# Optimization experiments

Measured on AMD Instinct MI355X. Metric: run time of the kernel, lower is better.

Reference implementation:

```python
import jax, jax.numpy as jnp
import numpy as np

NUM_PARTITIONS = 128
C = 32
D = 128
B, S, K = 4, 2048, 2


def setup_inputs() -> dict:
    key = jax.random.key(0)
    k1, k2, k3, k4 = jax.random.split(key, 4)
    partition_indices = jax.random.randint(k1, (B, S, K), 0, NUM_PARTITIONS)
    keys = jax.random.normal(k2, (B, S, K, C), dtype=jnp.float32)
    values = jax.random.normal(k3, (B, S, D), dtype=jnp.float32)
    queries = jax.random.normal(k4, (B, S, D), dtype=jnp.float32)
    return {
        "partition_indices": partition_indices,
        "keys": keys,
        "values": values,
        "queries": queries,
    }


def reference(partition_indices, keys, values, queries):
    # States start at zero; update() scatter-adds outer(k_bti, v_bt) into
    # states[p_bti]. read() then computes sum_i states[p_bti].mean(axis=0) * q_bt.
    b, s, k, c = keys.shape
    d = values.shape[-1]
    # outer products: [B,S,K,c,d]
    outer = keys[..., :, None] * values[:, :, None, None, :]
    flat_outer = outer.reshape(b * s * k, c, d)
    seg = partition_indices.reshape(-1)
    # scatter-add into partitioned states [P, c, d]
    states = jax.ops.segment_sum(flat_outer, seg, num_segments=NUM_PARTITIONS)
    means = states.mean(axis=1)  # [P, d]
    gathered = means[partition_indices]  # [B, S, K, d]
    out = gathered.sum(axis=2) * queries  # [B, S, d]
    return out
```

## Files before the change

### kernel.cpp

```cpp
#include <hip/hip_runtime.h>
#include <hip/hip_bf16.h>

#define P_  128
#define C_  32
#define D_  128
#define BS_ 8192
#define PD_ (P_*D_)
#define NB_MAX 256

__global__ __launch_bounds__(256) void scatter_partials(
    const int* __restrict__ idx, const float* __restrict__ keys,
    const float* __restrict__ values, float* __restrict__ partials,
    int rowsPerBlk)
{
    __shared__ float lmeans[PD_];
    const int tid  = threadIdx.x;
    for (int i = tid; i < PD_; i += 256) lmeans[i] = 0.f;
    __syncthreads();

    const int lane = tid & 63;
    const int wave = tid >> 6;
    const int r0 = blockIdx.x * rowsPerBlk;
    int r1 = r0 + rowsPerBlk; if (r1 > BS_) r1 = BS_;

    for (int r = r0 + wave; r < r1; r += 4) {
        const float kv = keys[(size_t)r * 64 + lane];
        const int i0 = idx[r * 2 + 0];
        const int i1 = idx[r * 2 + 1];
        const float va = values[(size_t)r * D_ + lane];
        const float vb = values[(size_t)r * D_ + 64 + lane];
        float s = kv;
        s += __shfl_xor(s, 16);
        s += __shfl_xor(s, 8);
        s += __shfl_xor(s, 4);
        s += __shfl_xor(s, 2);
        s += __shfl_xor(s, 1);
        const float ks0 = __shfl(s, 0)  * (1.f / 32.f);
        const float ks1 = __shfl(s, 32) * (1.f / 32.f);
        atomicAdd(&lmeans[i0 * D_ + lane],      ks0 * va);
        atomicAdd(&lmeans[i0 * D_ + 64 + lane], ks0 * vb);
        atomicAdd(&lmeans[i1 * D_ + lane],      ks1 * va);
        atomicAdd(&lmeans[i1 * D_ + 64 + lane], ks1 * vb);
    }
    __syncthreads();

    float4* dst = (float4*)(partials + (size_t)blockIdx.x * PD_);
    const float4* src = (const float4*)lmeans;
    for (int i = tid; i < PD_ / 4; i += 256) dst[i] = src[i];
}

__global__ __launch_bounds__(256) void reduce_partials(
    const float* __restrict__ partials, float* __restrict__ means, int nb)
{
    const int i = blockIdx.x * 256 + threadIdx.x;
    float s = 0.f;
    #pragma unroll 8
    for (int b = 0; b < nb; ++b) s += partials[(size_t)b * PD_ + i];
    means[i] = s;
}

__global__ __launch_bounds__(256) void emit_out(
    const int* __restrict__ idx, const float* __restrict__ means,
    const float* __restrict__ queries, float* __restrict__ out)
{
    const int gid = blockIdx.x * 256 + threadIdx.x;
    const int row = gid >> 5;
    const int d4  = gid & 31;
    const int i0 = idx[row * 2 + 0];
    const int i1 = idx[row * 2 + 1];
    const float4 q = ((const float4*)queries)[gid];
    const float4* m4 = (const float4*)means;
    const float4 a = m4[i0 * 32 + d4];
    const float4 b = m4[i1 * 32 + d4];
    float4 o;
    o.x = (a.x + b.x) * q.x;
    o.y = (a.y + b.y) * q.y;
    o.z = (a.z + b.z) * q.z;
    o.w = (a.w + b.w) * q.w;
    ((float4*)out)[gid] = o;
}

extern "C" void kernel_launch(void* const* d_in, const int* in_sizes, int n_in,
                              void* d_out, int out_size, void* d_ws, size_t ws_size,
                              hipStream_t stream) {
    const int*   idx     = (const int*)d_in[0];
    const float* keys    = (const float*)d_in[1];
    const float* values  = (const float*)d_in[2];
    const float* queries = (const float*)d_in[3];
    float* out = (float*)d_out;
    float* ws = (float*)d_ws;

    size_t slots = ws_size / (PD_ * sizeof(float));
    int nb = (int)slots - 1;
    if (nb > NB_MAX) nb = NB_MAX;
    if (nb < 1)      nb = 1;
    float* partials = ws;
    float* means    = ws + (size_t)nb * PD_;
    const int rowsPerBlk = (BS_ + nb - 1) / nb;

    scatter_partials<<<nb, 256, 0, stream>>>(idx, keys, values, partials, rowsPerBlk);
    reduce_partials<<<PD_ / 256, 256, 0, stream>>>(partials, means, nb);
    emit_out<<<(BS_ * D_ / 4) / 256, 256, 0, stream>>>(idx, means, queries, out);
}
```

Measured before the change: 105.1 us.

## Fix block count, batch row loads in scatter, split partial reduction across waves

Hardcodes 256 scatter blocks of 512 threads (8 waves), each wave loading its 4 rows up front so the global loads are in flight together before the LDS atomics. The reduce kernel now gives each element four waves, each summing 64 partials, and combines them in shared memory, which raises memory-level parallelism across 4x more blocks. Index loads are vectorised as int2. Dropping the workspace-size check assumes the workspace always holds 257 PD slots, and that may fail if it is smaller.

```diff
diff --git a/kernel.cpp b/kernel.cpp
--- a/kernel.cpp
+++ b/kernel.cpp
@@ -6,30 +6,36 @@
 #define D_  128
 #define BS_ 8192
 #define PD_ (P_*D_)
-#define NB_MAX 256
+#define NB_ 256
 
-__global__ __launch_bounds__(256) void scatter_partials(
+__global__ __launch_bounds__(512) void scatter_partials(
     const int* __restrict__ idx, const float* __restrict__ keys,
-    const float* __restrict__ values, float* __restrict__ partials,
-    int rowsPerBlk)
+    const float* __restrict__ values, float* __restrict__ partials)
 {
     __shared__ float lmeans[PD_];
-    const int tid  = threadIdx.x;
-    for (int i = tid; i < PD_; i += 256) lmeans[i] = 0.f;
+    float4* lm4 = (float4*)lmeans;
+    const int tid = threadIdx.x;
+    for (int i = tid; i < PD_ / 4; i += 512) lm4[i] = float4{0.f, 0.f, 0.f, 0.f};
     __syncthreads();
 
     const int lane = tid & 63;
     const int wave = tid >> 6;
-    const int r0 = blockIdx.x * rowsPerBlk;
-    int r1 = r0 + rowsPerBlk; if (r1 > BS_) r1 = BS_;
+    const int rbase = blockIdx.x * 32 + wave;
 
-    for (int r = r0 + wave; r < r1; r += 4) {
-        const float kv = keys[(size_t)r * 64 + lane];
-        const int i0 = idx[r * 2 + 0];
-        const int i1 = idx[r * 2 + 1];
-        const float va = values[(size_t)r * D_ + lane];
-        const float vb = values[(size_t)r * D_ + 64 + lane];
-        float s = kv;
+    float kv[4], va[4], vb[4];
+    int2  ii[4];
+    #pragma unroll
+    for (int j = 0; j < 4; ++j) {
+        const int r = rbase + 8 * j;
+        kv[j] = keys[(size_t)r * 64 + lane];
+        ii[j] = ((const int2*)idx)[r];
+        va[j] = values[(size_t)r * D_ + lane];
+        vb[j] = values[(size_t)r * D_ + 64 + lane];
+    }
+
+    #pragma unroll
+    for (int j = 0; j < 4; ++j) {
+        float s = kv[j];
         s += __shfl_xor(s, 16);
         s += __shfl_xor(s, 8);
         s += __shfl_xor(s, 4);
@@ -37,26 +43,33 @@
         s += __shfl_xor(s, 1);
         const float ks0 = __shfl(s, 0)  * (1.f / 32.f);
         const float ks1 = __shfl(s, 32) * (1.f / 32.f);
-        atomicAdd(&lmeans[i0 * D_ + lane],      ks0 * va);
-        atomicAdd(&lmeans[i0 * D_ + 64 + lane], ks0 * vb);
-        atomicAdd(&lmeans[i1 * D_ + lane],      ks1 * va);
-        atomicAdd(&lmeans[i1 * D_ + 64 + lane], ks1 * vb);
+        atomicAdd(&lmeans[ii[j].x * D_ + lane],      ks0 * va[j]);
+        atomicAdd(&lmeans[ii[j].x * D_ + 64 + lane], ks0 * vb[j]);
+        atomicAdd(&lmeans[ii[j].y * D_ + lane],      ks1 * va[j]);
+        atomicAdd(&lmeans[ii[j].y * D_ + 64 + lane], ks1 * vb[j]);
     }
     __syncthreads();
 
     float4* dst = (float4*)(partials + (size_t)blockIdx.x * PD_);
-    const float4* src = (const float4*)lmeans;
-    for (int i = tid; i < PD_ / 4; i += 256) dst[i] = src[i];
+    for (int i = tid; i < PD_ / 4; i += 512) dst[i] = lm4[i];
 }
 
 __global__ __launch_bounds__(256) void reduce_partials(
-    const float* __restrict__ partials, float* __restrict__ means, int nb)
+    const float* __restrict__ partials, float* __restrict__ means)
 {
-    const int i = blockIdx.x * 256 + threadIdx.x;
+    __shared__ float red[4][64];
+    const int t  = threadIdx.x;
+    const int el = t & 63;
+    const int g  = t >> 6;
+    const int e  = blockIdx.x * 64 + el;
     float s = 0.f;
     #pragma unroll 8
-    for (int b = 0; b < nb; ++b) s += partials[(size_t)b * PD_ + i];
-    means[i] = s;
+    for (int j = 0; j < 64; ++j)
+        s += partials[(size_t)(g * 64 + j) * PD_ + e];
+    red[g][el] = s;
+    __syncthreads();
+    if (t < 64)
+        means[blockIdx.x * 64 + t] = red[0][t] + red[1][t] + red[2][t] + red[3][t];
 }
 
 __global__ __launch_bounds__(256) void emit_out(
@@ -66,12 +79,11 @@
     const int gid = blockIdx.x * 256 + threadIdx.x;
     const int row = gid >> 5;
     const int d4  = gid & 31;
-    const int i0 = idx[row * 2 + 0];
-    const int i1 = idx[row * 2 + 1];
+    const int2 ii = ((const int2*)idx)[row];
     const float4 q = ((const float4*)queries)[gid];
     const float4* m4 = (const float4*)means;
-    const float4 a = m4[i0 * 32 + d4];
-    const float4 b = m4[i1 * 32 + d4];
+    const float4 a = m4[ii.x * 32 + d4];
+    const float4 b = m4[ii.y * 32 + d4];
     float4 o;
     o.x = (a.x + b.x) * q.x;
     o.y = (a.y + b.y) * q.y;
@@ -88,17 +100,12 @@
     const float* values  = (const float*)d_in[2];
     const float* queries = (const float*)d_in[3];
     float* out = (float*)d_out;
-    float* ws = (float*)d_ws;
+    float* ws  = (float*)d_ws;
 
-    size_t slots = ws_size / (PD_ * sizeof(float));
-    int nb = (int)slots - 1;
-    if (nb > NB_MAX) nb = NB_MAX;
-    if (nb < 1)      nb = 1;
     float* partials = ws;
-    float* means    = ws + (size_t)nb * PD_;
-    const int rowsPerBlk = (BS_ + nb - 1) / nb;
+    float* means    = ws + (size_t)NB_ * PD_;
 
-    scatter_partials<<<nb, 256, 0, stream>>>(idx, keys, values, partials, rowsPerBlk);
-    reduce_partials<<<PD_ / 256, 256, 0, stream>>>(partials, means, nb);
+    scatter_partials<<<NB_, 512, 0, stream>>>(idx, keys, values, partials);
+    reduce_partials<<<PD_ / 64, 256, 0, stream>>>(partials, means);
     emit_out<<<(BS_ * D_ / 4) / 256, 256, 0, stream>>>(idx, means, queries, out);
 }
```

Result: faster. 88.12 us (median of 2 runs) (-16.1%).
